# Optimization experiments

Hardware: AMD Instinct MI355X
Metric: run time of the kernel (lower is better)

The kernel has to match this reference:

```python
import jax, jax.numpy as jnp
import numpy as np

KH, KW = 3, 3           # kernel size
WS = KH * KW            # window_size = 9
PAD = 1                 # conv padding


def setup_inputs() -> dict:
    key = jax.random.key(0)
    k1, k2, k3 = jax.random.split(key, 3)
    x = jax.nn.relu(jax.random.normal(k1, (8, 64, 112, 112), dtype=jnp.float32))
    weight = jax.random.normal(k2, (64, 64, KH, KW), dtype=jnp.float32) * 0.05
    bias = jax.random.normal(k3, (64,), dtype=jnp.float32) * 0.05
    return {"x": x, "weight": weight, "bias": bias}


def _extract_patches(x):
    # x: (B, C, H, W) -> patches (B, C, H_out, W_out, KH, KW), stride 1, pad 1
    B, C, H, W = x.shape
    xp = jnp.pad(x, ((0, 0), (0, 0), (PAD, PAD), (PAD, PAD)))
    Hout, Wout = H, W  # stride 1, 'same' padding for 3x3
    cols = [xp[:, :, i:i + Hout, j:j + Wout] for i in range(KH) for j in range(KW)]
    return jnp.stack(cols, axis=-1).reshape(B, C, Hout, Wout, KH, KW)


def _zero_histogram(patches, weight):
    # Faithful to WindowDataCollector._update_hist: for every (batch, out_channel,
    # window, in_channel), multiply the 3x3 patch by the weights, count zeros in the
    # 9-element product, and histogram the zero-count per in_channel.
    # Scan over out_channels to avoid materializing the full (B,O,C,H,W,9) tensor
    # (mirrors the original spatial tiling; sums commute so result is identical).
    B, C = patches.shape[0], patches.shape[1]
    flat = patches  # (B, C, H, W, KH, KW)

    def step(hist, w_oc):  # w_oc: (C, KH, KW)
        prod = flat * w_oc[None, :, None, None, :, :]
        zeros = WS - jnp.count_nonzero(prod, axis=(-2, -1))      # (B, C, H, W) int
        zc = zeros.transpose(1, 0, 2, 3).reshape(C, -1)          # (C, B*H*W)
        h = jax.vmap(lambda z: jnp.bincount(z, length=WS + 1))(zc)
        return hist + h.astype(jnp.float32), None

    hist0 = jnp.zeros((C, WS + 1), jnp.float32)
    hist, _ = jax.lax.scan(step, hist0, weight)
    return hist


def reference(x, weight, bias):
    conv = jax.lax.conv_general_dilated(
        x, weight, window_strides=(1, 1), padding=[(PAD, PAD), (PAD, PAD)],
        dimension_numbers=("NCHW", "OIHW", "NCHW")) + bias[None, :, None, None]
    patches = _extract_patches(x)
    hist = _zero_histogram(patches, weight)  # (in_channels, window_size+1)
    return conv, hist
```

## Files before the change

kernel.cpp:

```cpp
#include <hip/hip_runtime.h>

typedef __attribute__((ext_vector_type(8))) short bf16x8;
typedef __attribute__((ext_vector_type(4))) float f32x4;

namespace {
constexpr int Bn = 8, Cn = 64, On = 64, Hn = 112, Wn = 112;
constexpr long CONV_ELEMS = (long)Bn * On * Hn * Wn;
constexpr int HP = 114, WP = 114;
constexpr long XT_ELEMS = (long)Bn * HP * WP * Cn;
constexpr size_t PART_BYTES = 20480;
constexpr size_t WB2_BYTES = 4 * 18 * 64 * 8 * 2;
constexpr size_t NEED_WS = PART_BYTES + (size_t)XT_ELEMS * 2 + WB2_BYTES;
constexpr int HIST_N = Cn * 10;
constexpr int HALO_PER_B = 2 * WP * Cn + 2 * Hn * Cn;
constexpr int HALO_ELEMS = Bn * HALO_PER_B;
constexpr int INT_BLOCKS = Bn * Hn * 2;
constexpr int HALO_BLOCKS = (HALO_ELEMS + 255) / 256;
constexpr int HIST_BLOCKS = Bn * Cn;
constexpr int WSETUP_BLOCKS = 64;
constexpr int PREP_GRID = HIST_BLOCKS + WSETUP_BLOCKS + INT_BLOCKS + HALO_BLOCKS;
constexpr int CONV_BLOCKS = Bn * 98;
constexpr int MAIN_GRID = CONV_BLOCKS + Cn;
}

__device__ __forceinline__ ushort f2bf(float v) {
    unsigned u = __float_as_uint(v);
    return (ushort)((u + 0x7fffu + ((u >> 16) & 1u)) >> 16);
}

__global__ __launch_bounds__(256) void prep_kernel(
    const float* __restrict__ x, const float* __restrict__ wt,
    ushort* __restrict__ xh, ushort* __restrict__ wb2, float* __restrict__ part)
{
    __shared__ __align__(16) char smem[14592];
    const int bx = blockIdx.x, tid = threadIdx.x;

    if (bx < HIST_BLOCKS) {
        unsigned* exm  = reinterpret_cast<unsigned*>(smem);
        int*      meta = reinterpret_cast<int*>(smem + 256);
        unsigned* wsum = reinterpret_cast<unsigned*>(smem + 264);
        unsigned* corr = reinterpret_cast<unsigned*>(smem + 352);
        const int b = bx >> 6, c = bx & 63;
        if (tid < 10) corr[tid] = 0u;
        if (tid < 64) {
            unsigned m = 0;
#pragma unroll
            for (int kp = 0; kp < 9; ++kp)
                if (wt[(tid * Cn + c) * 9 + kp] == 0.0f) m |= 1u << kp;
            exm[tid] = m;
            unsigned long long nz = __ballot(m == 0u);
            if (tid == 0) { meta[0] = (int)__popcll(nz); meta[1] = (nz != ~0ull); }
        }
        __syncthreads();

        const int h = tid >> 7;
        const int r = tid & 127;
        unsigned pk0 = 0, pk1 = 0;
        if (r < Hn) {
            const float* xp = x + ((long)b * Cn + c) * (Hn * Wn);
            auto rowmask = [&](int row) -> unsigned long long {
                if ((unsigned)row >= (unsigned)Hn) return (1ull << 58) - 1ull;
                const float* rp = xp + row * Wn;
                unsigned long long m;
                if (h == 0) {
                    m = 1ull;
#pragma unroll
                    for (int q = 0; q < 14; ++q) {
                        float4 v = *(const float4*)(rp + 4 * q);
                        unsigned nib = (unsigned)(v.x == 0.0f) | ((unsigned)(v.y == 0.0f) << 1)
                                     | ((unsigned)(v.z == 0.0f) << 2) | ((unsigned)(v.w == 0.0f) << 3);
                        m |= (unsigned long long)nib << (4 * q + 1);
                    }
                    m |= (unsigned long long)(rp[56] == 0.0f) << 57;
                } else {
                    m = (rp[55] == 0.0f) ? 1ull : 0ull;
#pragma unroll
                    for (int q = 0; q < 14; ++q) {
                        float4 v = *(const float4*)(rp + 56 + 4 * q);
                        unsigned nib = (unsigned)(v.x == 0.0f) | ((unsigned)(v.y == 0.0f) << 1)
                                     | ((unsigned)(v.z == 0.0f) << 2) | ((unsigned)(v.w == 0.0f) << 3);
                        m |= (unsigned long long)nib << (4 * q + 1);
                    }
                    m |= 1ull << 57;
                }
                return m;
            };
            unsigned long long Tm = rowmask(r - 1);
            unsigned long long Mm = rowmask(r);
            unsigned long long Bm = rowmask(r + 1);
#pragma unroll
            for (int i = 0; i < 56; ++i) {
                int z = __popc((unsigned)(Tm >> i) & 7u) + __popc((unsigned)(Mm >> i) & 7u)
                      + __popc((unsigned)(Bm >> i) & 7u);
                if (z < 5) pk0 += 1u << (6 * z); else pk1 += 1u << (6 * (z - 5));
            }
            if (meta[1]) {
                for (int i = 0; i < 56; ++i) {
                    unsigned m9 = ((unsigned)(Tm >> i) & 7u)
                                | (((unsigned)(Mm >> i) & 7u) << 3)
                                | (((unsigned)(Bm >> i) & 7u) << 6);
                    for (int oc = 0; oc < 64; ++oc)
                        if (exm[oc]) atomicAdd(&corr[__popc(m9 | exm[oc])], 1u);
                }
            }
        }
        unsigned s0 = (pk0 & 63u)         | ((pk0 >> 6 & 63u) << 16);
        unsigned s1 = (pk0 >> 12 & 63u)   | ((pk0 >> 18 & 63u) << 16);
        unsigned s2 = (pk0 >> 24 & 63u)   | ((pk1 & 63u) << 16);
        unsigned s3 = (pk1 >> 6 & 63u)    | ((pk1 >> 12 & 63u) << 16);
        unsigned s4 = (pk1 >> 18 & 63u)   | ((pk1 >> 24 & 63u) << 16);
#pragma unroll
        for (int l = 1; l < 64; l <<= 1) {
            s0 += __shfl_xor(s0, l); s1 += __shfl_xor(s1, l);
            s2 += __shfl_xor(s2, l); s3 += __shfl_xor(s3, l);
            s4 += __shfl_xor(s4, l);
        }
        const int wv = tid >> 6;
        if ((tid & 63) == 0) {
            wsum[wv * 5 + 0] = s0; wsum[wv * 5 + 1] = s1; wsum[wv * 5 + 2] = s2;
            wsum[wv * 5 + 3] = s3; wsum[wv * 5 + 4] = s4;
        }
        __syncthreads();
        if (tid < 10) {
            unsigned tot = 0;
#pragma unroll
            for (int w2 = 0; w2 < 4; ++w2)
                tot += (wsum[w2 * 5 + (tid >> 1)] >> ((tid & 1) * 16)) & 0xffffu;
            part[bx * 10 + tid] = (float)(tot * (unsigned)meta[0] + corr[tid]);
        }
        return;
    }

    int bx2 = bx - HIST_BLOCKS;
    if (bx2 < WSETUP_BLOCKS) {
        const int bw = bx2;
        for (int i = tid; i < 576; i += 256) {
            int flat = bw * 576 + i;
            int g = flat / 9216;
            int rem = flat - g * 9216;
            int k = rem >> 9;
            int rem2 = rem & 511;
            int lane = rem2 >> 3, j = rem2 & 7;
            int kk = k * 32 + (lane >> 4) * 8 + j;
            int kp = kk >> 6, cc = kk & 63;
            wb2[flat] = f2bf(wt[((g * 16 + (lane & 15)) * Cn + cc) * 9 + kp]);
        }
        return;
    }
    bx2 -= WSETUP_BLOCKS;
    if (bx2 < INT_BLOCKS) {
        auto ls = reinterpret_cast<float(*)[57]>(smem);
        const int b = bx2 / 224;
        const int rem = bx2 - b * 224;
        const int h = rem >> 1;
        const int w0 = (rem & 1) * 56;
        for (int i = tid; i < 64 * 56; i += 256) {
            int c = i / 56, w = i - c * 56;
            ls[c][w] = x[(((long)b * Cn + c) * Hn + h) * Wn + w0 + w];
        }
        __syncthreads();
        for (int i = tid; i < 56 * 64; i += 256) {
            int w = i >> 6, c = i & 63;
            xh[(((long)b * HP + h + 1) * WP + (w0 + w + 1)) * 64 + c] = f2bf(ls[c][w]);
        }
        return;
    }
    bx2 -= INT_BLOCKS;
    int idx = bx2 * 256 + tid;
    if (idx < HALO_ELEMS) {
        int b = idx / HALO_PER_B;
        int r = idx - b * HALO_PER_B;
        int h, w, cc;
        if (r < WP * Cn)                    { h = 0;      w = r / Cn;               cc = r & 63; }
        else if (r < 2 * WP * Cn)           { int q = r - WP * Cn; h = HP - 1; w = q / Cn; cc = q & 63; }
        else if (r < 2 * WP * Cn + Hn * Cn) { int q = r - 2 * WP * Cn; h = 1 + q / Cn; w = 0; cc = q & 63; }
        else                                { int q = r - 2 * WP * Cn - Hn * Cn; h = 1 + q / Cn; w = WP - 1; cc = q & 63; }
        xh[((long)(b * HP + h) * WP + w) * 64 + cc] = 0;
    }
}

__global__ __launch_bounds__(256, 4) void conv_kernel(
    const ushort* __restrict__ xh, const ushort* __restrict__ wb2,
    const float* __restrict__ bias, const float* __restrict__ part,
    float* __restrict__ out, float* __restrict__ hist)
{
    __shared__ __align__(16) ushort xs[11520];
    const int tid = threadIdx.x;

    if (blockIdx.x >= CONV_BLOCKS) {
        const int c = (int)blockIdx.x - CONV_BLOCKS;
        if (tid < 10) {
            float s = 0.0f;
#pragma unroll
            for (int b2 = 0; b2 < Bn; ++b2)
                s += part[(b2 * 64 + c) * 10 + tid];
            hist[c * 10 + tid] = s;
        }
        return;
    }

    int bid = (int)blockIdx.x;
    bid = (bid & 7) * 98 + (bid >> 3);
    const int b = bid / 98;
    const int t = bid - b * 98;
    const int h0 = (t / 7) * 8, w0 = (t % 7) * 16;
    const int lane = tid & 63, wvi = tid >> 6;
    const int l15 = lane & 15, lg = lane >> 4;
    const int pxh = wvi >> 1, och = wvi & 1;

    const ushort* xbase = xh + (long)((b * HP + h0) * WP + w0) * 64;
#pragma unroll
    for (int it = 0; it < 6; ++it) {
        int F = it * 256 + tid;
        if (F < 1440) {
            int R = F >> 3, p = F & 7;
            int hl = R / 18, wl = R - hl * 18;
            bf16x8 v = *(const bf16x8*)(xbase + (hl * WP + wl) * 64 + (p ^ (wl & 7)) * 8);
            *(bf16x8*)(xs + F * 8) = v;
        }
    }
    __syncthreads();

    const ushort* Bw0 = wb2 + (((och * 2 + 0) * 1152 + lane) << 3);
    const ushort* Bw1 = wb2 + (((och * 2 + 1) * 1152 + lane) << 3);
    f32x4 acc[4][2];
#pragma unroll
    for (int a = 0; a < 4; ++a)
#pragma unroll
        for (int j = 0; j < 2; ++j) acc[a][j] = (f32x4){0.f, 0.f, 0.f, 0.f};

    auto lda = [&](int k, bf16x8* A) {
        int kp = k >> 1, ch = k & 1;
        int dh = kp / 3, dw = kp - 3 * dh;
        int wl = l15 + dw;
        int rowb = pxh * 9216 + dh * 2304 + wl * 128;
        int colb = ((lg + 4 * ch) << 4) ^ ((wl & 7) << 4);
#pragma unroll
        for (int a = 0; a < 4; ++a)
            A[a] = *(const bf16x8*)((const char*)xs + a * 2304 + rowb + colb);
    };

    bf16x8 AX[4], AY[4], BX0, BX1, BY0, BY1;
    lda(0, AX);
    BX0 = *(const bf16x8*)(Bw0 + 0 * 512);
    BX1 = *(const bf16x8*)(Bw1 + 0 * 512);

#pragma unroll 1
    for (int t2 = 0; t2 < 9; ++t2) {
        BY0 = *(const bf16x8*)(Bw0 + (2 * t2 + 1) * 512);
        BY1 = *(const bf16x8*)(Bw1 + (2 * t2 + 1) * 512);
        lda(2 * t2 + 1, AY);
#pragma unroll
        for (int a = 0; a < 4; ++a)
            acc[a][0] = __builtin_amdgcn_mfma_f32_16x16x32_bf16(AX[a], BX0, acc[a][0], 0, 0, 0);
#pragma unroll
        for (int a = 0; a < 4; ++a)
            acc[a][1] = __builtin_amdgcn_mfma_f32_16x16x32_bf16(AX[a], BX1, acc[a][1], 0, 0, 0);
        const int kn = (t2 < 8) ? 2 * t2 + 2 : 17;
        BX0 = *(const bf16x8*)(Bw0 + kn * 512);
        BX1 = *(const bf16x8*)(Bw1 + kn * 512);
        lda(kn, AX);
#pragma unroll
        for (int a = 0; a < 4; ++a)
            acc[a][0] = __builtin_amdgcn_mfma_f32_16x16x32_bf16(AY[a], BY0, acc[a][0], 0, 0, 0);
#pragma unroll
        for (int a = 0; a < 4; ++a)
            acc[a][1] = __builtin_amdgcn_mfma_f32_16x16x32_bf16(AY[a], BY1, acc[a][1], 0, 0, 0);
    }

#pragma unroll
    for (int j = 0; j < 2; ++j) {
        const int oc = och * 32 + j * 16 + l15;
        const float bv = bias[oc];
#pragma unroll
        for (int a = 0; a < 4; ++a) {
            const int hr = h0 + pxh * 4 + a;
            float4 st = {acc[a][j].x + bv, acc[a][j].y + bv,
                         acc[a][j].z + bv, acc[a][j].w + bv};
            *reinterpret_cast<float4*>(
                out + (((long)b * On + oc) * Hn + hr) * Wn + w0 + lg * 4) = st;
        }
    }
}

namespace fb {
constexpr int TH = 8, TW = 16, CC = 8, NCH = Cn / CC;
constexpr int XROWS = TH + 2, XCOLS = TW + 2, XSTR = 20, WPAD = 68;
}
__global__ void setup_fb_kernel(const float* __restrict__ wt, float* __restrict__ hist,
                                int* __restrict__ n0, int* __restrict__ exCnt,
                                int* __restrict__ exMask) {
    int c = threadIdx.x;
    if (c >= Cn) return;
    int cnt0 = 0, ce = 0;
    for (int oc = 0; oc < On; ++oc) {
        unsigned m = 0;
        const float* wp = wt + (oc * Cn + c) * 9;
        for (int k = 0; k < 9; ++k)
            if (wp[k] == 0.0f) m |= (1u << k);
        if (m == 0u) ++cnt0;
        else exMask[c * 64 + (ce++)] = (int)m;
    }
    n0[c] = cnt0;
    exCnt[c] = ce;
    for (int j = 0; j < 10; ++j) hist[c * 10 + j] = 0.0f;
}
__global__ __launch_bounds__(256, 4) void conv_hist_kernel(
    const float* __restrict__ x, const float* __restrict__ wt,
    const float* __restrict__ bias, float* __restrict__ out,
    float* __restrict__ hist, const int* __restrict__ n0,
    const int* __restrict__ exCnt, const int* __restrict__ exMask)
{
    using namespace fb;
    __shared__ __align__(16) float xs[CC][XROWS][XSTR];
    __shared__ __align__(16) float ws[CC][9][WPAD];
    __shared__ unsigned hist_s[HIST_N];
    const int tid = threadIdx.x;
    const int bx = blockIdx.x;
    const int b = bx / 98;
    const int tt = bx - b * 98;
    const int h0 = (tt / 7) * TH;
    const int w0 = (tt % 7) * TW;
    const int ocg = tid >> 4, pg = tid & 15;
    const int prow = pg >> 1, pcol = (pg & 1) * 8;
    float acc[4][8];
#pragma unroll
    for (int o = 0; o < 4; ++o)
#pragma unroll
        for (int p = 0; p < 8; ++p) acc[o][p] = 0.0f;
    for (int i = tid; i < HIST_N; i += 256) hist_s[i] = 0u;
#pragma unroll 1
    for (int cc = 0; cc < NCH; ++cc) {
        const int cbase = cc * CC;
        __syncthreads();
#pragma unroll 1
        for (int i = tid; i < CC * XROWS * XCOLS; i += 256) {
            int c = i / (XROWS * XCOLS);
            int r = (i - c * XROWS * XCOLS) / XCOLS;
            int cl = i - c * XROWS * XCOLS - r * XCOLS;
            int gr = h0 - 1 + r, gc = w0 - 1 + cl;
            float v = 0.0f;
            if ((unsigned)gr < (unsigned)Hn && (unsigned)gc < (unsigned)Wn)
                v = x[(((long)b * Cn + cbase + c) * Hn + gr) * Wn + gc];
            xs[c][r][cl] = v;
        }
#pragma unroll 1
        for (int i = tid; i < On * CC * 9; i += 256) {
            int oc = i / (CC * 9);
            int j = i - oc * (CC * 9);
            int c = j / 9;
            int k = j - c * 9;
            ws[c][k][oc] = wt[(oc * Cn + cbase + c) * 9 + k];
        }
        __syncthreads();
#pragma unroll 1
        for (int c = 0; c < CC; ++c) {
#pragma unroll
            for (int kh = 0; kh < 3; ++kh) {
                const float* xrow = &xs[c][prow + kh][pcol];
                float4 xa = *(const float4*)xrow;
                float4 xb = *(const float4*)(xrow + 4);
                float2 xc = *(const float2*)(xrow + 8);
                float xr[10] = {xa.x, xa.y, xa.z, xa.w,
                                xb.x, xb.y, xb.z, xb.w, xc.x, xc.y};
#pragma unroll
                for (int kw = 0; kw < 3; ++kw) {
                    float4 wv = *(const float4*)&ws[c][kh * 3 + kw][ocg * 4];
                    float wr[4] = {wv.x, wv.y, wv.z, wv.w};
#pragma unroll
                    for (int o = 0; o < 4; ++o)
#pragma unroll
                        for (int p = 0; p < 8; ++p)
                            acc[o][p] = fmaf(wr[o], xr[p + kw], acc[o][p]);
                }
            }
        }
        if (tid < CC * 16) {
            const int c = tid >> 4;
            const int g = tid & 15;
            const int hr = g >> 1;
            const int hcb = (g & 1) * 8;
            unsigned rm[3];
#pragma unroll
            for (int kh = 0; kh < 3; ++kh) {
                const float* xrow = &xs[c][hr + kh][hcb];
                float4 xa = *(const float4*)xrow;
                float4 xb = *(const float4*)(xrow + 4);
                float2 xc = *(const float2*)(xrow + 8);
                unsigned m = 0;
                m |= (xa.x == 0.0f) ? 1u : 0u;
                m |= (xa.y == 0.0f) ? 2u : 0u;
                m |= (xa.z == 0.0f) ? 4u : 0u;
                m |= (xa.w == 0.0f) ? 8u : 0u;
                m |= (xb.x == 0.0f) ? 16u : 0u;
                m |= (xb.y == 0.0f) ? 32u : 0u;
                m |= (xb.z == 0.0f) ? 64u : 0u;
                m |= (xb.w == 0.0f) ? 128u : 0u;
                m |= (xc.x == 0.0f) ? 256u : 0u;
                m |= (xc.y == 0.0f) ? 512u : 0u;
                rm[kh] = m;
            }
            const int cg = cbase + c;
            const unsigned inc = (unsigned)n0[cg];
            const int ec = exCnt[cg];
#pragma unroll
            for (int j = 0; j < 8; ++j) {
                unsigned m9 = ((rm[0] >> j) & 7u)
                            | (((rm[1] >> j) & 7u) << 3)
                            | (((rm[2] >> j) & 7u) << 6);
                atomicAdd(&hist_s[cg * 10 + __popc(m9)], inc);
                for (int e = 0; e < ec; ++e) {
                    unsigned wz = (unsigned)exMask[cg * 64 + e];
                    atomicAdd(&hist_s[cg * 10 + __popc(m9 | wz)], 1u);
                }
            }
        }
    }
#pragma unroll
    for (int o = 0; o < 4; ++o) {
        const int oc = ocg * 4 + o;
        const float bv = bias[oc];
        float4 v0, v1;
        v0.x = acc[o][0] + bv; v0.y = acc[o][1] + bv;
        v0.z = acc[o][2] + bv; v0.w = acc[o][3] + bv;
        v1.x = acc[o][4] + bv; v1.y = acc[o][5] + bv;
        v1.z = acc[o][6] + bv; v1.w = acc[o][7] + bv;
        float* dst = &out[(((long)b * On + oc) * Hn + (h0 + prow)) * Wn + w0 + pcol];
        *(float4*)dst = v0;
        *(float4*)(dst + 4) = v1;
    }
    __syncthreads();
    for (int i = tid; i < HIST_N; i += 256)
        atomicAdd(&hist[i], (float)hist_s[i]);
}

extern "C" void kernel_launch(void* const* d_in, const int* in_sizes, int n_in,
                              void* d_out, int out_size, void* d_ws, size_t ws_size,
                              hipStream_t stream) {
    const float* x    = (const float*)d_in[0];
    const float* wt   = (const float*)d_in[1];
    const float* bias = (const float*)d_in[2];
    float* out  = (float*)d_out;
    float* hist = out + CONV_ELEMS;

    if (ws_size >= NEED_WS) {
        float*  part = (float*)d_ws;
        ushort* xh   = (ushort*)((char*)d_ws + PART_BYTES);
        ushort* wb2  = xh + XT_ELEMS;
        prep_kernel<<<PREP_GRID, 256, 0, stream>>>(x, wt, xh, wb2, part);
        conv_kernel<<<MAIN_GRID, 256, 0, stream>>>(xh, wb2, bias, part, out, hist);
    } else {
        int* n0     = (int*)d_ws;
        int* exCnt  = n0 + 64;
        int* exMask = n0 + 128;
        setup_fb_kernel<<<1, 64, 0, stream>>>(wt, hist, n0, exCnt, exMask);
        conv_hist_kernel<<<Bn * 98, 256, 0, stream>>>(x, wt, bias, out, hist,
                                                      n0, exCnt, exMask);
    }
}
```

Measured before the change: 41.90 us.

## Move zero-histogram blocks from prep kernel into conv kernel grid

The histogram-counting blocks now run as extra blocks of the conv kernel instead of the prep kernel, so their scalar work can overlap with the MFMA convolution rather than lengthen the prep phase. The per-batch partial buffer and the separate reduction blocks are replaced by float atomicAdds into the output histogram, which prep now zeroes. The conv kernel's launch bound is raised from 4 to 6 waves per SIMD, which caps registers per thread more tightly and may cause spills. The histogram blocks can still trail the conv blocks and extend the tail.

```diff
diff --git a/kernel.cpp b/kernel.cpp
--- a/kernel.cpp
+++ b/kernel.cpp
@@ -8,19 +8,18 @@
 constexpr long CONV_ELEMS = (long)Bn * On * Hn * Wn;
 constexpr int HP = 114, WP = 114;
 constexpr long XT_ELEMS = (long)Bn * HP * WP * Cn;
-constexpr size_t PART_BYTES = 20480;
 constexpr size_t WB2_BYTES = 4 * 18 * 64 * 8 * 2;
-constexpr size_t NEED_WS = PART_BYTES + (size_t)XT_ELEMS * 2 + WB2_BYTES;
+constexpr size_t NEED_WS = (size_t)XT_ELEMS * 2 + WB2_BYTES;
 constexpr int HIST_N = Cn * 10;
 constexpr int HALO_PER_B = 2 * WP * Cn + 2 * Hn * Cn;
 constexpr int HALO_ELEMS = Bn * HALO_PER_B;
 constexpr int INT_BLOCKS = Bn * Hn * 2;
 constexpr int HALO_BLOCKS = (HALO_ELEMS + 255) / 256;
+constexpr int WSETUP_BLOCKS = 64;
+constexpr int PREP_GRID = WSETUP_BLOCKS + INT_BLOCKS + HALO_BLOCKS;
+constexpr int CONV_BLOCKS = Bn * 98;
 constexpr int HIST_BLOCKS = Bn * Cn;
-constexpr int WSETUP_BLOCKS = 64;
-constexpr int PREP_GRID = HIST_BLOCKS + WSETUP_BLOCKS + INT_BLOCKS + HALO_BLOCKS;
-constexpr int CONV_BLOCKS = Bn * 98;
-constexpr int MAIN_GRID = CONV_BLOCKS + Cn;
+constexpr int MAIN_GRID = CONV_BLOCKS + HIST_BLOCKS;
 }
 
 __device__ __forceinline__ ushort f2bf(float v) {
@@ -30,17 +29,76 @@
 
 __global__ __launch_bounds__(256) void prep_kernel(
     const float* __restrict__ x, const float* __restrict__ wt,
-    ushort* __restrict__ xh, ushort* __restrict__ wb2, float* __restrict__ part)
+    ushort* __restrict__ xh, ushort* __restrict__ wb2, float* __restrict__ hist)
 {
     __shared__ __align__(16) char smem[14592];
     const int bx = blockIdx.x, tid = threadIdx.x;
 
-    if (bx < HIST_BLOCKS) {
+    if (bx < WSETUP_BLOCKS) {
+        const int bw = bx;
+        for (int i = tid; i < 576; i += 256) {
+            int flat = bw * 576 + i;
+            int g = flat / 9216;
+            int rem = flat - g * 9216;
+            int k = rem >> 9;
+            int rem2 = rem & 511;
+            int lane = rem2 >> 3, j = rem2 & 7;
+            int kk = k * 32 + (lane >> 4) * 8 + j;
+            int kp = kk >> 6, cc = kk & 63;
+            wb2[flat] = f2bf(wt[((g * 16 + (lane & 15)) * Cn + cc) * 9 + kp]);
+        }
+        if (bw == 0)
+            for (int i = tid; i < HIST_N; i += 256) hist[i] = 0.0f;
+        return;
+    }
+
+    int bx2 = bx - WSETUP_BLOCKS;
+    if (bx2 < INT_BLOCKS) {
+        auto ls = reinterpret_cast<float(*)[57]>(smem);
+        const int b = bx2 / 224;
+        const int rem = bx2 - b * 224;
+        const int h = rem >> 1;
+        const int w0 = (rem & 1) * 56;
+        for (int i = tid; i < 64 * 56; i += 256) {
+            int c = i / 56, w = i - c * 56;
+            ls[c][w] = x[(((long)b * Cn + c) * Hn + h) * Wn + w0 + w];
+        }
+        __syncthreads();
+        for (int i = tid; i < 56 * 64; i += 256) {
+            int w = i >> 6, c = i & 63;
+            xh[(((long)b * HP + h + 1) * WP + (w0 + w + 1)) * 64 + c] = f2bf(ls[c][w]);
+        }
+        return;
+    }
+    bx2 -= INT_BLOCKS;
+    int idx = bx2 * 256 + tid;
+    if (idx < HALO_ELEMS) {
+        int b = idx / HALO_PER_B;
+        int r = idx - b * HALO_PER_B;
+        int h, w, cc;
+        if (r < WP * Cn)                    { h = 0;      w = r / Cn;               cc = r & 63; }
+        else if (r < 2 * WP * Cn)           { int q = r - WP * Cn; h = HP - 1; w = q / Cn; cc = q & 63; }
+        else if (r < 2 * WP * Cn + Hn * Cn) { int q = r - 2 * WP * Cn; h = 1 + q / Cn; w = 0; cc = q & 63; }
+        else                                { int q = r - 2 * WP * Cn - Hn * Cn; h = 1 + q / Cn; w = WP - 1; cc = q & 63; }
+        xh[((long)(b * HP + h) * WP + w) * 64 + cc] = 0;
+    }
+}
+
+__global__ __launch_bounds__(256, 6) void conv_kernel(
+    const ushort* __restrict__ xh, const ushort* __restrict__ wb2,
+    const float* __restrict__ bias, const float* __restrict__ x,
+    const float* __restrict__ wt, float* __restrict__ out, float* __restrict__ hist)
+{
+    __shared__ __align__(16) char smem[23040];
+    const int tid = threadIdx.x;
+
+    if (blockIdx.x >= CONV_BLOCKS) {
         unsigned* exm  = reinterpret_cast<unsigned*>(smem);
         int*      meta = reinterpret_cast<int*>(smem + 256);
         unsigned* wsum = reinterpret_cast<unsigned*>(smem + 264);
         unsigned* corr = reinterpret_cast<unsigned*>(smem + 352);
-        const int b = bx >> 6, c = bx & 63;
+        const int hb = (int)blockIdx.x - CONV_BLOCKS;
+        const int b = hb >> 6, c = hb & 63;
         if (tid < 10) corr[tid] = 0u;
         if (tid < 64) {
             unsigned m = 0;
@@ -104,11 +162,11 @@
                 }
             }
         }
-        unsigned s0 = (pk0 & 63u)         | ((pk0 >> 6 & 63u) << 16);
-        unsigned s1 = (pk0 >> 12 & 63u)   | ((pk0 >> 18 & 63u) << 16);
-        unsigned s2 = (pk0 >> 24 & 63u)   | ((pk1 & 63u) << 16);
-        unsigned s3 = (pk1 >> 6 & 63u)    | ((pk1 >> 12 & 63u) << 16);
-        unsigned s4 = (pk1 >> 18 & 63u)   | ((pk1 >> 24 & 63u) << 16);
+        unsigned s0 = (pk0 & 63u)       | ((pk0 >> 6 & 63u) << 16);
+        unsigned s1 = (pk0 >> 12 & 63u) | ((pk0 >> 18 & 63u) << 16);
+        unsigned s2 = (pk0 >> 24 & 63u) | ((pk1 & 63u) << 16);
+        unsigned s3 = (pk1 >> 6 & 63u)  | ((pk1 >> 12 & 63u) << 16);
+        unsigned s4 = (pk1 >> 18 & 63u) | ((pk1 >> 24 & 63u) << 16);
 #pragma unroll
         for (int l = 1; l < 64; l <<= 1) {
             s0 += __shfl_xor(s0, l); s1 += __shfl_xor(s1, l);
@@ -126,79 +184,12 @@
 #pragma unroll
             for (int w2 = 0; w2 < 4; ++w2)
                 tot += (wsum[w2 * 5 + (tid >> 1)] >> ((tid & 1) * 16)) & 0xffffu;
-            part[bx * 10 + tid] = (float)(tot * (unsigned)meta[0] + corr[tid]);
+            atomicAdd(&hist[c * 10 + tid], (float)(tot * (unsigned)meta[0] + corr[tid]));
         }
         return;
     }
 
-    int bx2 = bx - HIST_BLOCKS;
-    if (bx2 < WSETUP_BLOCKS) {
-        const int bw = bx2;
-        for (int i = tid; i < 576; i += 256) {
-            int flat = bw * 576 + i;
-            int g = flat / 9216;
-            int rem = flat - g * 9216;
-            int k = rem >> 9;
-            int rem2 = rem & 511;
-            int lane = rem2 >> 3, j = rem2 & 7;
-            int kk = k * 32 + (lane >> 4) * 8 + j;
-            int kp = kk >> 6, cc = kk & 63;
-            wb2[flat] = f2bf(wt[((g * 16 + (lane & 15)) * Cn + cc) * 9 + kp]);
-        }
-        return;
-    }
-    bx2 -= WSETUP_BLOCKS;
-    if (bx2 < INT_BLOCKS) {
-        auto ls = reinterpret_cast<float(*)[57]>(smem);
-        const int b = bx2 / 224;
-        const int rem = bx2 - b * 224;
-        const int h = rem >> 1;
-        const int w0 = (rem & 1) * 56;
-        for (int i = tid; i < 64 * 56; i += 256) {
-            int c = i / 56, w = i - c * 56;
-            ls[c][w] = x[(((long)b * Cn + c) * Hn + h) * Wn + w0 + w];
-        }
-        __syncthreads();
-        for (int i = tid; i < 56 * 64; i += 256) {
-            int w = i >> 6, c = i & 63;
-            xh[(((long)b * HP + h + 1) * WP + (w0 + w + 1)) * 64 + c] = f2bf(ls[c][w]);
-        }
-        return;
-    }
-    bx2 -= INT_BLOCKS;
-    int idx = bx2 * 256 + tid;
-    if (idx < HALO_ELEMS) {
-        int b = idx / HALO_PER_B;
-        int r = idx - b * HALO_PER_B;
-        int h, w, cc;
-        if (r < WP * Cn)                    { h = 0;      w = r / Cn;               cc = r & 63; }
-        else if (r < 2 * WP * Cn)           { int q = r - WP * Cn; h = HP - 1; w = q / Cn; cc = q & 63; }
-        else if (r < 2 * WP * Cn + Hn * Cn) { int q = r - 2 * WP * Cn; h = 1 + q / Cn; w = 0; cc = q & 63; }
-        else                                { int q = r - 2 * WP * Cn - Hn * Cn; h = 1 + q / Cn; w = WP - 1; cc = q & 63; }
-        xh[((long)(b * HP + h) * WP + w) * 64 + cc] = 0;
-    }
-}
-
-__global__ __launch_bounds__(256, 4) void conv_kernel(
-    const ushort* __restrict__ xh, const ushort* __restrict__ wb2,
-    const float* __restrict__ bias, const float* __restrict__ part,
-    float* __restrict__ out, float* __restrict__ hist)
-{
-    __shared__ __align__(16) ushort xs[11520];
-    const int tid = threadIdx.x;
-
-    if (blockIdx.x >= CONV_BLOCKS) {
-        const int c = (int)blockIdx.x - CONV_BLOCKS;
-        if (tid < 10) {
-            float s = 0.0f;
-#pragma unroll
-            for (int b2 = 0; b2 < Bn; ++b2)
-                s += part[(b2 * 64 + c) * 10 + tid];
-            hist[c * 10 + tid] = s;
-        }
-        return;
-    }
-
+    ushort* xs = (ushort*)smem;
     int bid = (int)blockIdx.x;
     bid = (bid & 7) * 98 + (bid >> 3);
     const int b = bid / 98;
@@ -444,11 +435,10 @@
     float* hist = out + CONV_ELEMS;
 
     if (ws_size >= NEED_WS) {
-        float*  part = (float*)d_ws;
-        ushort* xh   = (ushort*)((char*)d_ws + PART_BYTES);
-        ushort* wb2  = xh + XT_ELEMS;
-        prep_kernel<<<PREP_GRID, 256, 0, stream>>>(x, wt, xh, wb2, part);
-        conv_kernel<<<MAIN_GRID, 256, 0, stream>>>(xh, wb2, bias, part, out, hist);
+        ushort* xh  = (ushort*)d_ws;
+        ushort* wb2 = xh + XT_ELEMS;
+        prep_kernel<<<PREP_GRID, 256, 0, stream>>>(x, wt, xh, wb2, hist);
+        conv_kernel<<<MAIN_GRID, 256, 0, stream>>>(xh, wb2, bias, x, wt, out, hist);
     } else {
         int* n0     = (int*)d_ws;
         int* exCnt  = n0 + 64;
```

After: 38.74 us (median of 2 runs). 7.5% less time.
